# Optimization experiments

Measured on AMD Instinct MI355X. Metric: run time of the kernel, lower is better.

## Reference

```python
import jax, jax.numpy as jnp
import numpy as np

B, S1, S2, D1, D2 = 4, 2048, 2048, 512, 512
H, DK, DV = 8, 64, 64


def setup_inputs() -> dict:
    key = jax.random.key(0)
    ks = jax.random.split(key, 8)
    x1 = jax.random.normal(ks[0], (B, S1, D1), dtype=jnp.float32)
    x2 = jax.random.normal(ks[1], (B, S2, D2), dtype=jnp.float32)
    x3 = jax.random.normal(ks[2], (B, S2, D2), dtype=jnp.float32)
    s = 0.02
    Wq = jax.random.normal(ks[3], (D1, H * DK), dtype=jnp.float32) * s
    Wk = jax.random.normal(ks[4], (D2, H * DK), dtype=jnp.float32) * s
    Wv = jax.random.normal(ks[5], (D2, H * DV), dtype=jnp.float32) * s
    Wo = jax.random.normal(ks[6], (H * DV, D1), dtype=jnp.float32) * s
    bo = jnp.zeros((D1,), dtype=jnp.float32)
    return {"x1": x1, "x2": x2, "x3": x3, "Wq": Wq, "Wk": Wk, "Wv": Wv, "Wo": Wo, "bo": bo}


def reference(x1, x2, x3, Wq, Wk, Wv, Wo, bo):
    b, s1, _ = x1.shape
    # project to per-head q, k, v: [B, H, S, Dh]
    q = (x1 @ Wq).reshape(b, s1, H, DK).transpose(0, 2, 1, 3)
    k = (x2 @ Wk).reshape(b, x2.shape[1], H, DK).transpose(0, 2, 1, 3)
    v = (x3 @ Wv).reshape(b, x3.shape[1], H, DV).transpose(0, 2, 1, 3)
    scores = jnp.einsum('bhqd,bhkd->bhqk', q, k) / jnp.sqrt(jnp.float32(DK))
    attn = jax.nn.softmax(scores, axis=-1)
    out = jnp.einsum('bhqk,bhkd->bhqd', attn, v)  # [B, H, S1, DV]
    out = out.transpose(0, 2, 1, 3).reshape(b, s1, H * DV)
    return out @ Wo + bo
```

## Files before the change

### kernel.cpp

```cpp
#include <hip/hip_runtime.h>

typedef __attribute__((ext_vector_type(4))) float f32x4;
typedef __attribute__((ext_vector_type(8))) __bf16 bf16x8;
typedef __attribute__((ext_vector_type(4))) __bf16 bf16x4;
typedef __attribute__((ext_vector_type(8))) _Float16 f16x8;
typedef __attribute__((ext_vector_type(4))) _Float16 f16x4;
typedef __attribute__((ext_vector_type(2))) __fp16 fp16x2;

#define DEVINL __device__ __forceinline__

DEVINL void gld16(const void* g, void* l) {
  __builtin_amdgcn_global_load_lds((__attribute__((address_space(1))) void*)(void*)g,
                                   (__attribute__((address_space(3))) void*)l, 16, 0, 0);
}

DEVINL f32x4 mfma32(bf16x8 a, bf16x8 b, f32x4 c) {
  return __builtin_amdgcn_mfma_f32_16x16x32_bf16(a, b, c, 0, 0, 0);
}
DEVINL f32x4 mfma16h(f16x4 a, f16x4 b, f32x4 c) {
  return __builtin_amdgcn_mfma_f32_16x16x16f16(a, b, c, 0, 0, 0);
}

DEVINL fp16x2 pk16(float a, float b) { return __builtin_amdgcn_cvt_pkrtz(a, b); }


__global__ __launch_bounds__(256) void cvt_all(const float* x1, const float* x2, const float* x3,
                                               const float* Wq, const float* Wk, const float* Wv,
                                               const float* Wo, __bf16* o0, __bf16* o1, __bf16* o2,
                                               __bf16* WT) {
  __shared__ float t[64][65];
  const int bx = blockIdx.x;
  if (bx < 12288) {
    const int z = bx >> 12;
    const float* s = z == 0 ? x1 : z == 1 ? x2 : x3;
    __bf16* d = z == 0 ? o0 : z == 1 ? o1 : o2;
    size_t i = (size_t)(bx & 4095) * 256 + threadIdx.x;
    f32x4 v = ((const f32x4*)s)[i];
    bf16x4 o;
#pragma unroll
    for (int j = 0; j < 4; ++j) o[j] = (__bf16)v[j];
    ((bf16x4*)d)[i] = o;
  } else {
    const int l = bx - 12288;
    const int z = l >> 6;
    const float* W = z == 0 ? Wq : z == 1 ? Wk : z == 2 ? Wv : Wo;
    __bf16* D = WT + (size_t)z * 512 * 512;
    const int r0 = ((l >> 3) & 7) * 64, c0 = (l & 7) * 64;
    const int tx = threadIdx.x & 63, ty = threadIdx.x >> 6;
#pragma unroll
    for (int j = 0; j < 16; ++j)
      t[ty + j * 4][tx] = W[(size_t)(r0 + ty + j * 4) * 512 + c0 + tx];
    __syncthreads();
#pragma unroll
    for (int j = 0; j < 16; ++j)
      D[(size_t)(c0 + ty + j * 4) * 512 + r0 + tx] = (__bf16)t[tx][ty + j * 4];
  }
}


DEVINL void gemm_tile(const __bf16* A, const __bf16* Bt, int m0, int n0,
                      __bf16* As, __bf16* Bs, f32x4 acc[4][4]) {
  const int tid = threadIdx.x, lane = tid & 63, w = tid >> 6;
  const int qd = lane >> 4, r = lane & 15;
  const int wm = w & 1, wn = w >> 1;
  const char* ap[4];
  const char* bp[4];
#pragma unroll
  for (int j = 0; j < 4; ++j) {
    int c = (w * 4 + j) * 64 + lane;
    int row = c >> 3, cs = c & 7;
    int gc = cs ^ (row & 7);
    ap[j] = (const char*)A + (size_t)(m0 + row) * 1024 + gc * 16;
    bp[j] = (const char*)Bt + (size_t)(n0 + row) * 1024 + gc * 16;
  }
  int offA[4][2], offB[4][2];
#pragma unroll
  for (int t = 0; t < 4; ++t)
#pragma unroll
    for (int ks = 0; ks < 2; ++ks) {
      int m = wm * 64 + t * 16 + r;
      offA[t][ks] = m * 128 + (((ks * 4 + qd) ^ (m & 7)) * 16);
      int n = wn * 64 + t * 16 + r;
      offB[t][ks] = n * 128 + (((ks * 4 + qd) ^ (n & 7)) * 16);
    }
  char* AsC = (char*)As;
  char* BsC = (char*)Bs;
  for (int kt = 0; kt < 8; ++kt) {
    __syncthreads();
#pragma unroll
    for (int j = 0; j < 4; ++j) {
      gld16(ap[j] + kt * 128, AsC + (w * 4 + j) * 1024);
      gld16(bp[j] + kt * 128, BsC + (w * 4 + j) * 1024);
    }
    __syncthreads();
#pragma unroll
    for (int ks = 0; ks < 2; ++ks) {
      bf16x8 a[4], b[4];
#pragma unroll
      for (int t = 0; t < 4; ++t) {
        a[t] = *(const bf16x8*)(AsC + offA[t][ks]);
        b[t] = *(const bf16x8*)(BsC + offB[t][ks]);
      }
#pragma unroll
      for (int i = 0; i < 4; ++i)
#pragma unroll
        for (int j2 = 0; j2 < 4; ++j2)
          acc[i][j2] = mfma32(a[i], b[j2], acc[i][j2]);
    }
  }
}

__global__ __launch_bounds__(256, 3) void gemm_proj(const __bf16* x1b, const __bf16* x2b,
                                                    const __bf16* x3b, const __bf16* WT,
                                                    __bf16* Qo, __bf16* Ko, _Float16* Vto) {
  __shared__ __align__(16) char smem[34816];
  __bf16* As = (__bf16*)smem;
  __bf16* Bs = (__bf16*)(smem + 16384);
  const int z = blockIdx.z;
  const __bf16* A = z == 0 ? x1b : z == 1 ? x2b : x3b;
  const __bf16* Bt = WT + (size_t)z * 512 * 512;
  const int l = blockIdx.x;
  const int sidx = l >> 3;
  const int m0 = ((l & 7) * 8 + (sidx >> 2)) * 128;
  const int n0 = (sidx & 3) * 128;
  f32x4 acc[4][4] = {};
  gemm_tile(A, Bt, m0, n0, As, Bs, acc);
  const int tid = threadIdx.x, lane = tid & 63, w = tid >> 6;
  const int qd = lane >> 4, r = lane & 15, wm = w & 1, wn = w >> 1;
  const int b = m0 >> 11, sbase = m0 & 2047;
  if (z == 2) {
    __syncthreads();
    char* T = smem;
#pragma unroll
    for (int mt = 0; mt < 4; ++mt)
#pragma unroll
      for (int nt = 0; nt < 4; ++nt) {
        int dv = wn * 64 + nt * 16 + r;
        int sl = wm * 64 + mt * 16 + qd * 4;
        f16x4 p4;
#pragma unroll
        for (int g = 0; g < 4; ++g) p4[g] = (_Float16)acc[mt][nt][g];
        *(f16x4*)(T + (size_t)dv * 272 + sl * 2) = p4;
      }
    __syncthreads();
#pragma unroll
    for (int p2 = 0; p2 < 2; ++p2) {
      int dvrow = p2 * 64 + (tid >> 2);
      int col = n0 + dvrow, h = col >> 6, d = col & 63;
      char* dst = (char*)(Vto + ((size_t)(b * 8 + h) * 64 + d) * 2048 + sbase) + (tid & 3) * 16;
#pragma unroll
      for (int j = 0; j < 4; ++j) {
        bf16x8 vv = *(const bf16x8*)(T + (size_t)dvrow * 272 + (tid & 3) * 16 + j * 64);
        *(bf16x8*)(dst + j * 64) = vv;
      }
    }
  } else {
    const float qscale = 0.18033688f;
#pragma unroll
    for (int mt = 0; mt < 4; ++mt) {
#pragma unroll
      for (int nt = 0; nt < 4; ++nt) {
        f32x4 v = acc[mt][nt];
        if (z == 0) {
#pragma unroll
          for (int g = 0; g < 4; ++g) v[g] *= qscale;
        }
        int col = n0 + wn * 64 + nt * 16 + r;
        int h = col >> 6, d = col & 63;
        int s = sbase + wm * 64 + mt * 16 + qd * 4;
        __bf16* O = (z == 0 ? Qo : Ko) + ((size_t)(b * 8 + h) * 2048 + s) * 64 + d;
#pragma unroll
        for (int g = 0; g < 4; ++g) O[(size_t)g * 64] = (__bf16)v[g];
      }
    }
  }
}

__global__ __launch_bounds__(256, 2) void gemm_out(const __bf16* Ob, const __bf16* WoT,
                                                   const float* bo, float* out) {
  __shared__ __align__(16) __bf16 As[64 * 64];
  __shared__ __align__(16) __bf16 Bs[128 * 64];
  const int tid = threadIdx.x, lane = tid & 63, w = tid >> 6;
  const int qd = lane >> 4, r = lane & 15, wm = w & 1, wn = w >> 1;
  const int id = blockIdx.x;
  const int rest = id >> 3;
  const int m0 = ((id & 7) * 16 + (rest & 15)) * 64;
  const int n0 = (rest >> 4) * 128;
  const char* ap[2];
  const char* bp[4];
#pragma unroll
  for (int j = 0; j < 2; ++j) {
    int c = (w * 2 + j) * 64 + lane;
    int row = c >> 3, gc = (c & 7) ^ (row & 7);
    ap[j] = (const char*)Ob + (size_t)(m0 + row) * 1024 + gc * 16;
  }
#pragma unroll
  for (int j = 0; j < 4; ++j) {
    int c = (w * 4 + j) * 64 + lane;
    int row = c >> 3, gc = (c & 7) ^ (row & 7);
    bp[j] = (const char*)WoT + (size_t)(n0 + row) * 1024 + gc * 16;
  }
  int offA[2][2], offB[4][2];
#pragma unroll
  for (int ks = 0; ks < 2; ++ks) {
#pragma unroll
    for (int t = 0; t < 2; ++t) {
      int m = wm * 32 + t * 16 + r;
      offA[t][ks] = m * 128 + (((ks * 4 + qd) ^ (m & 7)) * 16);
    }
#pragma unroll
    for (int t = 0; t < 4; ++t) {
      int n = wn * 64 + t * 16 + r;
      offB[t][ks] = n * 128 + (((ks * 4 + qd) ^ (n & 7)) * 16);
    }
  }
  char* AsC = (char*)As;
  char* BsC = (char*)Bs;
  f32x4 acc[2][4] = {};
  for (int kt = 0; kt < 8; ++kt) {
    __syncthreads();
#pragma unroll
    for (int j = 0; j < 2; ++j) gld16(ap[j] + kt * 128, AsC + (w * 2 + j) * 1024);
#pragma unroll
    for (int j = 0; j < 4; ++j) gld16(bp[j] + kt * 128, BsC + (w * 4 + j) * 1024);
    __syncthreads();
#pragma unroll
    for (int ks = 0; ks < 2; ++ks) {
      bf16x8 a[2], b[4];
#pragma unroll
      for (int t = 0; t < 2; ++t) a[t] = *(const bf16x8*)(AsC + offA[t][ks]);
#pragma unroll
      for (int t = 0; t < 4; ++t) b[t] = *(const bf16x8*)(BsC + offB[t][ks]);
#pragma unroll
      for (int i = 0; i < 2; ++i)
#pragma unroll
        for (int j2 = 0; j2 < 4; ++j2)
          acc[i][j2] = mfma32(a[i], b[j2], acc[i][j2]);
    }
  }
#pragma unroll
  for (int nt = 0; nt < 4; ++nt) {
    int col = n0 + wn * 64 + nt * 16 + r;
    float bv = bo[col];
#pragma unroll
    for (int mt = 0; mt < 2; ++mt) {
      int mg = m0 + wm * 32 + mt * 16 + qd * 4;
#pragma unroll
      for (int g = 0; g < 4; ++g) out[(size_t)(mg + g) * 512 + col] = acc[mt][nt][g] + bv;
    }
  }
}

__global__ __launch_bounds__(256, 4) void attn(const __bf16* Q, const __bf16* K,
                                               const _Float16* Vt, _Float16* Opart, float* Lp) {
  __shared__ __align__(16) __bf16 Qs[128 * 64];
  __shared__ __align__(16) __bf16 Ks[64 * 64];
  __shared__ __align__(16) _Float16 Vs[64 * 64];
  const int tid = threadIdx.x, lane = tid & 63, w = tid >> 6;
  const int qd = lane >> 4, r = lane & 15;
  const int id = blockIdx.x;
  const int rest = id >> 3;
  const int bh = (id & 7) * 4 + (rest >> 5);
  const int kvh = (rest >> 4) & 1;
  const int q0 = (rest & 15) * 128;
  const __bf16* Qg = Q + ((size_t)bh * 2048 + q0) * 64;
  const __bf16* Kg = K + (size_t)bh * 2048 * 64;
  const _Float16* Vg = Vt + (size_t)bh * 64 * 2048;
  char* QsC = (char*)Qs;
  char* KsC = (char*)Ks;
  char* VsC = (char*)Vs;

#pragma unroll
  for (int j = 0; j < 4; ++j) {
    int c = (w * 4 + j) * 64 + lane;
    int m = c >> 3, gc = (c & 7) ^ (m & 7);
    gld16((const char*)Qg + m * 128 + gc * 16, QsC + (w * 4 + j) * 1024);
  }
  __syncthreads();

  bf16x8 qf[2][2];
#pragma unroll
  for (int mt = 0; mt < 2; ++mt)
#pragma unroll
    for (int ks = 0; ks < 2; ++ks) {
      int m = w * 32 + mt * 16 + r;
      qf[mt][ks] = *(const bf16x8*)(QsC + m * 128 + (((ks * 4 + qd) ^ (m & 7)) * 16));
    }

  int offK[4][2];
  int offV[4][4];
#pragma unroll
  for (int t = 0; t < 4; ++t) {
    int n = t * 16 + r;
#pragma unroll
    for (int ks = 0; ks < 2; ++ks) offK[t][ks] = n * 128 + (((ks * 4 + qd) ^ (n & 7)) * 16);
#pragma unroll
    for (int nt = 0; nt < 4; ++nt)
      offV[t][nt] = n * 128 + (((2 * nt + (qd >> 1)) ^ (n & 7)) * 16) + (qd & 1) * 8;
  }

  const f16x4 ones = {(_Float16)1.f, (_Float16)1.f, (_Float16)1.f, (_Float16)1.f};
  f32x4 oacc[2][4] = {};
  f32x4 lacc[2] = {};

  const int kt0 = kvh * 16;
  for (int kt = kt0; kt < kt0 + 16; ++kt) {
    __syncthreads();
#pragma unroll
    for (int j = 0; j < 2; ++j) {
      int c = (w * 2 + j) * 64 + lane;
      int m = c >> 3, gc = (c & 7) ^ (m & 7);
      gld16((const char*)Kg + (size_t)(kt * 64 + m) * 128 + gc * 16, KsC + (w * 2 + j) * 1024);
      gld16((const char*)Vg + (size_t)m * 4096 + kt * 128 + gc * 16, VsC + (w * 2 + j) * 1024);
    }
    __syncthreads();

    f32x4 sf[2][4] = {};
#pragma unroll
    for (int nt = 0; nt < 4; ++nt) {
      bf16x8 kf0 = *(const bf16x8*)(KsC + offK[nt][0]);
      bf16x8 kf1 = *(const bf16x8*)(KsC + offK[nt][1]);
#pragma unroll
      for (int mt = 0; mt < 2; ++mt) {
        sf[mt][nt] = mfma32(kf0, qf[mt][0], sf[mt][nt]);
        sf[mt][nt] = mfma32(kf1, qf[mt][1], sf[mt][nt]);
      }
    }
    f16x4 pf[2][4];
#pragma unroll
    for (int mt = 0; mt < 2; ++mt)
#pragma unroll
      for (int nt = 0; nt < 4; ++nt) {
        fp16x2 lo = pk16(__builtin_exp2f(sf[mt][nt][0]), __builtin_exp2f(sf[mt][nt][1]));
        fp16x2 hi = pk16(__builtin_exp2f(sf[mt][nt][2]), __builtin_exp2f(sf[mt][nt][3]));
        f16x4 p;
        p[0] = (_Float16)lo[0];
        p[1] = (_Float16)lo[1];
        p[2] = (_Float16)hi[0];
        p[3] = (_Float16)hi[1];
        pf[mt][nt] = p;
        lacc[mt] = mfma16h(ones, p, lacc[mt]);
      }
#pragma unroll
    for (int dvt = 0; dvt < 4; ++dvt) {
      f16x4 vf[4];
#pragma unroll
      for (int nt = 0; nt < 4; ++nt) vf[nt] = *(const f16x4*)(VsC + offV[dvt][nt]);
#pragma unroll
      for (int mt = 0; mt < 2; ++mt)
#pragma unroll
        for (int nt = 0; nt < 4; ++nt)
          oacc[mt][dvt] = mfma16h(vf[nt], pf[mt][nt], oacc[mt][dvt]);
    }
  }

  const size_t pbase = (size_t)(kvh * 32 + bh) * 2048;
#pragma unroll
  for (int mt = 0; mt < 2; ++mt)
    if (lane < 16) Lp[pbase + q0 + w * 32 + mt * 16 + r] = lacc[mt][0];
  _Float16* Ob0 = Opart + pbase * 64;
#pragma unroll
  for (int mt = 0; mt < 2; ++mt) {
    const int s = q0 + w * 32 + mt * 16 + r;
#pragma unroll
    for (int dvt = 0; dvt < 4; ++dvt) {
      f16x4 o4;
#pragma unroll
      for (int g = 0; g < 4; ++g) o4[g] = (_Float16)oacc[mt][dvt][g];
      *(f16x4*)(Ob0 + (size_t)s * 64 + dvt * 16 + qd * 4) = o4;
    }
  }
}

__global__ __launch_bounds__(256) void combine(const _Float16* Op, const float* Lp, __bf16* Ob) {
  int c = blockIdx.x * 256 + threadIdx.x;
  int bhs = c >> 3;
  int dv0 = (c & 7) * 8;
  size_t e = (size_t)bhs * 64 + dv0;
  f16x8 a = *(const f16x8*)(Op + e);
  f16x8 b2 = *(const f16x8*)(Op + ((size_t)32 * 2048 * 64) + e);
  float inv = 1.0f / (Lp[bhs] + Lp[bhs + 65536]);
  int bh = bhs >> 11, s = bhs & 2047, b = bh >> 3, h = bh & 7;
  bf16x8 o;
#pragma unroll
  for (int j = 0; j < 8; ++j) o[j] = (__bf16)(((float)a[j] + (float)b2[j]) * inv);
  *(bf16x8*)(Ob + ((size_t)(b * 2048 + s)) * 512 + h * 64 + dv0) = o;
}


extern "C" void kernel_launch(void* const* d_in, const int* in_sizes, int n_in,
                              void* d_out, int out_size, void* d_ws, size_t ws_size,
                              hipStream_t stream) {
  const float* x1 = (const float*)d_in[0];
  const float* x2 = (const float*)d_in[1];
  const float* x3 = (const float*)d_in[2];
  const float* Wq = (const float*)d_in[3];
  const float* Wk = (const float*)d_in[4];
  const float* Wv = (const float*)d_in[5];
  const float* Wo = (const float*)d_in[6];
  const float* bo = (const float*)d_in[7];
  float* out = (float*)d_out;
  char* ws = (char*)d_ws;
  const size_t MB = 1ull << 20;
  __bf16* x1b = (__bf16*)(ws);
  __bf16* x2b = (__bf16*)(ws + 8 * MB);
  __bf16* x3b = (__bf16*)(ws + 16 * MB);
  __bf16* WT = (__bf16*)(ws + 24 * MB);
  __bf16* Qb = (__bf16*)(ws + 26 * MB);
  __bf16* Kb = (__bf16*)(ws + 34 * MB);
  _Float16* Vtb = (_Float16*)(ws + 42 * MB);
  __bf16* Ob = (__bf16*)(ws + 50 * MB);
  _Float16* Opart = (_Float16*)(ws + 58 * MB);
  float* Lp = (float*)(ws + 75 * MB);

  cvt_all<<<dim3(12544), 256, 0, stream>>>(x1, x2, x3, Wq, Wk, Wv, Wo, x1b, x2b, x3b, WT);
  gemm_proj<<<dim3(256, 1, 3), 256, 0, stream>>>(x1b, x2b, x3b, WT, Qb, Kb, Vtb);
  attn<<<dim3(1024), 256, 0, stream>>>(Qb, Kb, Vtb, Opart, Lp);
  combine<<<dim3(2048), 256, 0, stream>>>(Opart, Lp, Ob);
  gemm_out<<<dim3(512), 256, 0, stream>>>(Ob, WT + 3ull * 512 * 512, bo, out);
}
```

Measured before the change: 198.2 us.

## Fuse split-KV combine into output GEMM and use packed fp16 polynomial exp2

Removes the separate combine kernel. The output projection GEMM now loads both fp16 partial attention outputs, sums them and scales by the reciprocal softmax denominator while building its A fragments, and multiplies against an fp16 copy of Wo. This drops the intermediate bf16 O buffer, its write and re-read, and one launch, at the cost of twice the A-tile loads and extra ALU work in the GEMM. Separately, the attention softmax replaces per-element exp2f with a packed half-precision polynomial exp2 built by exponent bit manipulation. That cuts transcendental cost but reduces accuracy, and the polynomial may misbehave for large-magnitude inputs.

Measured after the change: 188.1 us. 5.1% less time.

```diff
diff --git a/kernel.cpp b/kernel.cpp
--- a/kernel.cpp
+++ b/kernel.cpp
@@ -5,7 +5,9 @@
 typedef __attribute__((ext_vector_type(4))) __bf16 bf16x4;
 typedef __attribute__((ext_vector_type(8))) _Float16 f16x8;
 typedef __attribute__((ext_vector_type(4))) _Float16 f16x4;
+typedef __attribute__((ext_vector_type(2))) _Float16 f16x2;
 typedef __attribute__((ext_vector_type(2))) __fp16 fp16x2;
+typedef __attribute__((ext_vector_type(2))) unsigned short u16x2;
 
 #define DEVINL __device__ __forceinline__
 
@@ -20,14 +22,32 @@
 DEVINL f32x4 mfma16h(f16x4 a, f16x4 b, f32x4 c) {
   return __builtin_amdgcn_mfma_f32_16x16x16f16(a, b, c, 0, 0, 0);
 }
+DEVINL f32x4 mfma32h(f16x8 a, f16x8 b, f32x4 c) {
+  return __builtin_amdgcn_mfma_f32_16x16x32_f16(a, b, c, 0, 0, 0);
+}
 
 DEVINL fp16x2 pk16(float a, float b) { return __builtin_amdgcn_cvt_pkrtz(a, b); }
+
+DEVINL f16x2 pexp2(f16x2 x) {
+  const f16x2 mag = {(_Float16)1536.f, (_Float16)1536.f};
+  const f16x2 c3 = {(_Float16)0.0555041f, (_Float16)0.0555041f};
+  const f16x2 c2 = {(_Float16)0.2402265f, (_Float16)0.2402265f};
+  const f16x2 c1 = {(_Float16)0.6931472f, (_Float16)0.6931472f};
+  const f16x2 one = {(_Float16)1.f, (_Float16)1.f};
+  f16x2 t = x + mag;
+  f16x2 f = x - (t - mag);
+  f16x2 p = c3 * f + c2;
+  p = p * f + c1;
+  p = p * f + one;
+  u16x2 n = (__builtin_bit_cast(u16x2, t) - (u16x2){0x6600, 0x6600}) << 10;
+  return __builtin_bit_cast(f16x2, (u16x2)(__builtin_bit_cast(u16x2, p) + n));
+}
 
 
 __global__ __launch_bounds__(256) void cvt_all(const float* x1, const float* x2, const float* x3,
                                                const float* Wq, const float* Wk, const float* Wv,
                                                const float* Wo, __bf16* o0, __bf16* o1, __bf16* o2,
-                                               __bf16* WT) {
+                                               __bf16* WT, _Float16* Wo16) {
   __shared__ float t[64][65];
   const int bx = blockIdx.x;
   if (bx < 12288) {
@@ -44,16 +64,22 @@
     const int l = bx - 12288;
     const int z = l >> 6;
     const float* W = z == 0 ? Wq : z == 1 ? Wk : z == 2 ? Wv : Wo;
-    __bf16* D = WT + (size_t)z * 512 * 512;
     const int r0 = ((l >> 3) & 7) * 64, c0 = (l & 7) * 64;
     const int tx = threadIdx.x & 63, ty = threadIdx.x >> 6;
 #pragma unroll
     for (int j = 0; j < 16; ++j)
       t[ty + j * 4][tx] = W[(size_t)(r0 + ty + j * 4) * 512 + c0 + tx];
     __syncthreads();
-#pragma unroll
-    for (int j = 0; j < 16; ++j)
-      D[(size_t)(c0 + ty + j * 4) * 512 + r0 + tx] = (__bf16)t[tx][ty + j * 4];
+    if (z == 3) {
+#pragma unroll
+      for (int j = 0; j < 16; ++j)
+        Wo16[(size_t)(c0 + ty + j * 4) * 512 + r0 + tx] = (_Float16)t[tx][ty + j * 4];
+    } else {
+      __bf16* D = WT + (size_t)z * 512 * 512;
+#pragma unroll
+      for (int j = 0; j < 16; ++j)
+        D[(size_t)(c0 + ty + j * 4) * 512 + r0 + tx] = (__bf16)t[tx][ty + j * 4];
+    }
   }
 }
 
@@ -176,29 +202,42 @@
   }
 }
 
-__global__ __launch_bounds__(256, 2) void gemm_out(const __bf16* Ob, const __bf16* WoT,
-                                                   const float* bo, float* out) {
-  __shared__ __align__(16) __bf16 As[64 * 64];
-  __shared__ __align__(16) __bf16 Bs[128 * 64];
+__global__ __launch_bounds__(256, 2) void gemm_out(const _Float16* Op, const float* Lp,
+                                                   const _Float16* Wo16, const float* bo,
+                                                   float* out) {
+  __shared__ __align__(16) _Float16 As1[64 * 64];
+  __shared__ __align__(16) _Float16 As2[64 * 64];
+  __shared__ __align__(16) _Float16 Bs[128 * 64];
   const int tid = threadIdx.x, lane = tid & 63, w = tid >> 6;
   const int qd = lane >> 4, r = lane & 15, wm = w & 1, wn = w >> 1;
   const int id = blockIdx.x;
   const int rest = id >> 3;
   const int m0 = ((id & 7) * 16 + (rest & 15)) * 64;
   const int n0 = (rest >> 4) * 128;
+  const int b = m0 >> 11, s2b = m0 & 2047;
+  _Float16 invh[2][8];
+#pragma unroll
+  for (int t = 0; t < 2; ++t) {
+    int s2 = s2b + wm * 32 + t * 16 + r;
+#pragma unroll
+    for (int h = 0; h < 8; ++h) {
+      float l = Lp[(size_t)(b * 8 + h) * 2048 + s2] + Lp[(size_t)(32 + b * 8 + h) * 2048 + s2];
+      invh[t][h] = (_Float16)(1.0f / l);
+    }
+  }
   const char* ap[2];
   const char* bp[4];
 #pragma unroll
   for (int j = 0; j < 2; ++j) {
     int c = (w * 2 + j) * 64 + lane;
-    int row = c >> 3, gc = (c & 7) ^ (row & 7);
-    ap[j] = (const char*)Ob + (size_t)(m0 + row) * 1024 + gc * 16;
+    int m = c >> 3, gc = (c & 7) ^ (m & 7);
+    ap[j] = (const char*)(Op + ((size_t)(b * 8) * 2048 + s2b + m) * 64 + gc * 8);
   }
 #pragma unroll
   for (int j = 0; j < 4; ++j) {
     int c = (w * 4 + j) * 64 + lane;
     int row = c >> 3, gc = (c & 7) ^ (row & 7);
-    bp[j] = (const char*)WoT + (size_t)(n0 + row) * 1024 + gc * 16;
+    bp[j] = (const char*)(Wo16 + (size_t)(n0 + row) * 512 + gc * 8);
   }
   int offA[2][2], offB[4][2];
 #pragma unroll
@@ -214,28 +253,42 @@
       offB[t][ks] = n * 128 + (((ks * 4 + qd) ^ (n & 7)) * 16);
     }
   }
-  char* AsC = (char*)As;
+  char* As1C = (char*)As1;
+  char* As2C = (char*)As2;
   char* BsC = (char*)Bs;
+  const size_t HSTRIDE = (size_t)2048 * 64 * 2;
+  const size_t HALF = (size_t)32 * 2048 * 64 * 2;
   f32x4 acc[2][4] = {};
+#pragma unroll
   for (int kt = 0; kt < 8; ++kt) {
     __syncthreads();
 #pragma unroll
-    for (int j = 0; j < 2; ++j) gld16(ap[j] + kt * 128, AsC + (w * 2 + j) * 1024);
+    for (int j = 0; j < 2; ++j) {
+      gld16(ap[j] + (size_t)kt * HSTRIDE, As1C + (w * 2 + j) * 1024);
+      gld16(ap[j] + (size_t)kt * HSTRIDE + HALF, As2C + (w * 2 + j) * 1024);
+    }
 #pragma unroll
     for (int j = 0; j < 4; ++j) gld16(bp[j] + kt * 128, BsC + (w * 4 + j) * 1024);
     __syncthreads();
 #pragma unroll
     for (int ks = 0; ks < 2; ++ks) {
-      bf16x8 a[2], b[4];
-#pragma unroll
-      for (int t = 0; t < 2; ++t) a[t] = *(const bf16x8*)(AsC + offA[t][ks]);
-#pragma unroll
-      for (int t = 0; t < 4; ++t) b[t] = *(const bf16x8*)(BsC + offB[t][ks]);
+      f16x8 a[2], bb[4];
+#pragma unroll
+      for (int t = 0; t < 2; ++t) {
+        f16x8 a1 = *(const f16x8*)(As1C + offA[t][ks]);
+        f16x8 a2 = *(const f16x8*)(As2C + offA[t][ks]);
+        f16x8 iv;
+#pragma unroll
+        for (int j = 0; j < 8; ++j) iv[j] = invh[t][kt];
+        a[t] = (a1 + a2) * iv;
+      }
+#pragma unroll
+      for (int t = 0; t < 4; ++t) bb[t] = *(const f16x8*)(BsC + offB[t][ks]);
 #pragma unroll
       for (int i = 0; i < 2; ++i)
 #pragma unroll
         for (int j2 = 0; j2 < 4; ++j2)
-          acc[i][j2] = mfma32(a[i], b[j2], acc[i][j2]);
+          acc[i][j2] = mfma32h(a[i], bb[j2], acc[i][j2]);
     }
   }
 #pragma unroll
@@ -331,13 +384,9 @@
     for (int mt = 0; mt < 2; ++mt)
 #pragma unroll
       for (int nt = 0; nt < 4; ++nt) {
-        fp16x2 lo = pk16(__builtin_exp2f(sf[mt][nt][0]), __builtin_exp2f(sf[mt][nt][1]));
-        fp16x2 hi = pk16(__builtin_exp2f(sf[mt][nt][2]), __builtin_exp2f(sf[mt][nt][3]));
-        f16x4 p;
-        p[0] = (_Float16)lo[0];
-        p[1] = (_Float16)lo[1];
-        p[2] = (_Float16)hi[0];
-        p[3] = (_Float16)hi[1];
+        f16x2 e01 = pexp2(__builtin_bit_cast(f16x2, pk16(sf[mt][nt][0], sf[mt][nt][1])));
+        f16x2 e23 = pexp2(__builtin_bit_cast(f16x2, pk16(sf[mt][nt][2], sf[mt][nt][3])));
+        f16x4 p = {e01[0], e01[1], e23[0], e23[1]};
         pf[mt][nt] = p;
         lacc[mt] = mfma16h(ones, p, lacc[mt]);
       }
@@ -370,21 +419,6 @@
       *(f16x4*)(Ob0 + (size_t)s * 64 + dvt * 16 + qd * 4) = o4;
     }
   }
-}
-
-__global__ __launch_bounds__(256) void combine(const _Float16* Op, const float* Lp, __bf16* Ob) {
-  int c = blockIdx.x * 256 + threadIdx.x;
-  int bhs = c >> 3;
-  int dv0 = (c & 7) * 8;
-  size_t e = (size_t)bhs * 64 + dv0;
-  f16x8 a = *(const f16x8*)(Op + e);
-  f16x8 b2 = *(const f16x8*)(Op + ((size_t)32 * 2048 * 64) + e);
-  float inv = 1.0f / (Lp[bhs] + Lp[bhs + 65536]);
-  int bh = bhs >> 11, s = bhs & 2047, b = bh >> 3, h = bh & 7;
-  bf16x8 o;
-#pragma unroll
-  for (int j = 0; j < 8; ++j) o[j] = (__bf16)(((float)a[j] + (float)b2[j]) * inv);
-  *(bf16x8*)(Ob + ((size_t)(b * 2048 + s)) * 512 + h * 64 + dv0) = o;
 }
 
 
@@ -409,13 +443,12 @@
   __bf16* Qb = (__bf16*)(ws + 26 * MB);
   __bf16* Kb = (__bf16*)(ws + 34 * MB);
   _Float16* Vtb = (_Float16*)(ws + 42 * MB);
-  __bf16* Ob = (__bf16*)(ws + 50 * MB);
-  _Float16* Opart = (_Float16*)(ws + 58 * MB);
-  float* Lp = (float*)(ws + 75 * MB);
-
-  cvt_all<<<dim3(12544), 256, 0, stream>>>(x1, x2, x3, Wq, Wk, Wv, Wo, x1b, x2b, x3b, WT);
+  _Float16* Opart = (_Float16*)(ws + 50 * MB);
+  float* Lp = (float*)(ws + 66 * MB);
+  _Float16* Wo16 = (_Float16*)(ws + 67 * MB);
+
+  cvt_all<<<dim3(12544), 256, 0, stream>>>(x1, x2, x3, Wq, Wk, Wv, Wo, x1b, x2b, x3b, WT, Wo16);
   gemm_proj<<<dim3(256, 1, 3), 256, 0, stream>>>(x1b, x2b, x3b, WT, Qb, Kb, Vtb);
   attn<<<dim3(1024), 256, 0, stream>>>(Qb, Kb, Vtb, Opart, Lp);
-  combine<<<dim3(2048), 256, 0, stream>>>(Opart, Lp, Ob);
-  gemm_out<<<dim3(512), 256, 0, stream>>>(Ob, WT + 3ull * 512 * 512, bo, out);
-}
+  gemm_out<<<dim3(512), 256, 0, stream>>>(Opart, Lp, Wo16, bo, out);
+}
```
